# Optimization experiments

Measured on AMD Instinct MI355X. Metric: run time of the kernel, lower is better.

The kernel has to match this reference:

```python
import jax, jax.numpy as jnp
import numpy as np

DIM = 512
HEADS = 8
HD = DIM // HEADS          # head_dim = 64
GROUPS = 32                # GroupNorm groups
EPS = 1e-5
SCALE = HD ** -0.25        # double-scale: applied to both q and k
B, H, W, L, CTX = 8, 32, 32, 77, 768


def setup_inputs() -> dict:
    key = jax.random.key(0)
    ks = jax.random.split(key, 6)
    return {
        "x": jax.random.normal(ks[0], (B, DIM, H, W), jnp.float32),
        "context": jax.random.normal(ks[1], (B, L, CTX), jnp.float32),
        "gn_gamma": jnp.ones((DIM,), jnp.float32),
        "gn_beta": jnp.zeros((DIM,), jnp.float32),
        "qkv_w": jax.random.normal(ks[2], (3 * DIM, DIM), jnp.float32) * 0.02,
        "qkv_b": jnp.zeros((3 * DIM,), jnp.float32),
        "ckv_w": jax.random.normal(ks[3], (2 * DIM, CTX), jnp.float32) * 0.02,
        "ckv_b": jnp.zeros((2 * DIM,), jnp.float32),
        "proj_w": jax.random.normal(ks[4], (DIM, DIM), jnp.float32) * 0.02,
        "proj_b": jnp.zeros((DIM,), jnp.float32),
    }


def _group_norm(x, gamma, beta):
    b, c, h, w = x.shape
    xr = x.reshape(b, GROUPS, c // GROUPS, h, w)
    mu = xr.mean(axis=(2, 3, 4), keepdims=True)
    var = xr.var(axis=(2, 3, 4), keepdims=True)
    xr = (xr - mu) * jax.lax.rsqrt(var + EPS)
    return xr.reshape(b, c, h, w) * gamma[None, :, None, None] + beta[None, :, None, None]


def reference(x, context, gn_gamma, gn_beta, qkv_w, qkv_b, ckv_w, ckv_b, proj_w, proj_b):
    b, c, h, w = x.shape
    n, d = HEADS, HD
    identity = x

    xn = _group_norm(x, gn_gamma, gn_beta)
    # 1x1 conv == channel GEMM. qkv: [b, 3*dim, h*w] -> [b, 3, n, d, hw]
    qkv = jnp.einsum('bchw,oc->bohw', xn, qkv_w) + qkv_b[None, :, None, None]
    qkv = qkv.reshape(b, 3, n, d, h * w)
    q, k, v = qkv[:, 0], qkv[:, 1], qkv[:, 2]   # each [b, n, d, hw]

    # context kv: Linear(context_dim, 2*dim) -> [b, L, 2, n, d] -> [b, n, d, L]
    ckv = jnp.einsum('blc,oc->blo', context, ckv_w) + ckv_b
    ckv = ckv.reshape(b, -1, 2, n, d)
    ck = jnp.transpose(ckv[:, :, 0], (0, 2, 3, 1))  # [b, n, d, L]
    cv = jnp.transpose(ckv[:, :, 1], (0, 2, 3, 1))
    k = jnp.concatenate([ck, k], axis=-1)           # [b, n, d, L+hw]
    v = jnp.concatenate([cv, v], axis=-1)

    # attn = (q^T * s) @ (k * s); softmax over keys
    attn = jnp.einsum('bndq,bndk->bnqk', q * SCALE, k * SCALE)
    attn = jax.nn.softmax(attn, axis=-1)
    out = jnp.einsum('bndk,bnqk->bndq', v, attn).reshape(b, c, h, w)

    out = jnp.einsum('bchw,oc->bohw', out, proj_w) + proj_b[None, :, None, None]
    return out + identity
```

## Files before the change

### kernel.cpp

```cpp
#include <hip/hip_runtime.h>

#define B_ 8
#define DIM_ 512
#define HEADS_ 8
#define HD_ 64
#define HW_ 1024
#define L_ 77
#define LP_ 80
#define CTX_ 768
#define KV_ 1101
#define KVP_ 1152
#define CTX0_ 1024
#define SC_QK 0.42466089f

typedef __attribute__((ext_vector_type(8))) short bf16x8;
typedef __attribute__((ext_vector_type(4))) float f32x4;
typedef __attribute__((ext_vector_type(4))) unsigned short u16x4;

__device__ __forceinline__ unsigned short f2bf(float f) {
  union { float f; unsigned int u; } c; c.f = f;
  unsigned int u = c.u;
  return (unsigned short)((u + 0x7fffu + ((u >> 16) & 1u)) >> 16);
}
__device__ __forceinline__ float bf2f(unsigned short h) {
  union { unsigned int u; float f; } c; c.u = ((unsigned int)h) << 16;
  return c.f;
}

#define GLD_LDS16(gsrc, ldst) \
  __builtin_amdgcn_global_load_lds((const __attribute__((address_space(1))) void*)(gsrc), \
                                   (__attribute__((address_space(3))) void*)(ldst), 16, 0, 0)

__global__ __launch_bounds__(256) void conv_w_k(const float* __restrict__ qkv_w,
                                                const float* __restrict__ ckv_w,
                                                const float* __restrict__ proj_w,
                                                unsigned short* __restrict__ dq,
                                                unsigned short* __restrict__ dc,
                                                unsigned short* __restrict__ dp) {
  int i = blockIdx.x * 256 + threadIdx.x;
  const float* src;
  unsigned short* dst;
  int off;
  if (i < 196608) { src = qkv_w; dst = dq; off = i; }
  else if (i < 393216) { src = ckv_w; dst = dc; off = i - 196608; }
  else { src = proj_w; dst = dp; off = i - 393216; }
  float4 v = *(const float4*)(src + (size_t)off * 4);
  u16x4 o;
  o[0] = f2bf(v.x); o[1] = f2bf(v.y); o[2] = f2bf(v.z); o[3] = f2bf(v.w);
  *(u16x4*)(dst + (size_t)off * 4) = o;
}

__global__ __launch_bounds__(256) void conv_ctx_k(const float* __restrict__ ctx,
                                                  unsigned short* __restrict__ dst) {
  int i = blockIdx.x * 256 + threadIdx.x;
  int total4 = B_ * LP_ * CTX_ / 4;
  if (i >= total4) return;
  int idx = i * 4;
  int b = idx / (LP_ * CTX_);
  int rem = idx - b * (LP_ * CTX_);
  int l = rem / CTX_;
  int c = rem - l * CTX_;
  float4 v = make_float4(0.f, 0.f, 0.f, 0.f);
  if (l < L_) v = *(const float4*)&ctx[((size_t)b * L_ + l) * CTX_ + c];
  u16x4 o;
  o[0] = f2bf(v.x); o[1] = f2bf(v.y); o[2] = f2bf(v.z); o[3] = f2bf(v.w);
  *(u16x4*)(dst + idx) = o;
}

__global__ __launch_bounds__(256) void pad_zero_k(unsigned short* __restrict__ k_s,
                                                  unsigned short* __restrict__ vT) {
  int i = blockIdx.x * 256 + threadIdx.x;
  const int total = 64 * (KVP_ - KV_) * 64;
  if (i >= total) return;
  int bh = i / ((KVP_ - KV_) * 64);
  int rem = i - bh * ((KVP_ - KV_) * 64);
  int row = KV_ + rem / 64;
  int d = rem & 63;
  k_s[((size_t)bh * KVP_ + row) * HD_ + d] = 0;
  vT[((size_t)bh * HD_ + d) * KVP_ + row] = 0;
}

__global__ __launch_bounds__(256) void gnorm_k(const float* __restrict__ x,
                                               const float* __restrict__ gamma,
                                               const float* __restrict__ beta,
                                               unsigned short* __restrict__ xn_t) {
  __shared__ unsigned short xs[16][1032];
  __shared__ float red[8];
  const int tid = threadIdx.x;
  const int b = blockIdx.x >> 5, g = blockIdx.x & 31;
  const float* xp = x + ((size_t)b * DIM_ + g * 16) * HW_;
  float sum = 0.f, ssq = 0.f;
#pragma unroll
  for (int i = 0; i < 16; ++i) {
    float4 v = *(const float4*)&xp[i * HW_ + tid * 4];
    sum += v.x + v.y + v.z + v.w;
    ssq += v.x * v.x + v.y * v.y + v.z * v.z + v.w * v.w;
    xs[i][tid * 4 + 0] = f2bf(v.x);
    xs[i][tid * 4 + 1] = f2bf(v.y);
    xs[i][tid * 4 + 2] = f2bf(v.z);
    xs[i][tid * 4 + 3] = f2bf(v.w);
  }
#pragma unroll
  for (int off = 32; off >= 1; off >>= 1) {
    sum += __shfl_xor(sum, off, 64);
    ssq += __shfl_xor(ssq, off, 64);
  }
  if ((tid & 63) == 0) { red[(tid >> 6) * 2] = sum; red[(tid >> 6) * 2 + 1] = ssq; }
  __syncthreads();
  sum = red[0] + red[2] + red[4] + red[6];
  ssq = red[1] + red[3] + red[5] + red[7];
  float mu = sum * (1.f / 16384.f);
  float rstd = rsqrtf(ssq * (1.f / 16384.f) - mu * mu + 1e-5f);
  float a[16], c[16];
#pragma unroll
  for (int ci = 0; ci < 16; ++ci) {
    float gm = gamma[g * 16 + ci], bt = beta[g * 16 + ci];
    a[ci] = rstd * gm;
    c[ci] = bt - mu * rstd * gm;
  }
#pragma unroll
  for (int t = 0; t < 4; ++t) {
    int hw = tid + t * 256;
    unsigned short tmp[16];
#pragma unroll
    for (int ci = 0; ci < 16; ++ci)
      tmp[ci] = f2bf(bf2f(xs[ci][hw]) * a[ci] + c[ci]);
    unsigned int w[8];
#pragma unroll
    for (int j = 0; j < 8; ++j) w[j] = (unsigned int)tmp[2 * j] | ((unsigned int)tmp[2 * j + 1] << 16);
    unsigned short* dptr = &xn_t[((size_t)b * HW_ + hw) * DIM_ + g * 16];
    *(uint4*)dptr = make_uint4(w[0], w[1], w[2], w[3]);
    *(uint4*)(dptr + 8) = make_uint4(w[4], w[5], w[6], w[7]);
  }
}

template <int MODE, int BM, int BN>
__device__ __forceinline__ void gemm_body(int bid,
                                          const unsigned short* __restrict__ A,
                                          const unsigned short* __restrict__ Bt,
                                          int M, int N, int K,
                                          const float* __restrict__ bias,
                                          unsigned short* __restrict__ out_q,
                                          unsigned short* __restrict__ out_k,
                                          unsigned short* __restrict__ out_v,
                                          const float* __restrict__ xres,
                                          float* __restrict__ outf,
                                          unsigned short* sm) {
  constexpr int MR = BM / 32;
  constexpr int NR = BN / 32;
  constexpr int SLOADS = BM / 32 + BN / 32;
  unsigned short* As0 = sm;
  unsigned short* Bs0 = sm + 2 * BM * 64;
  const int tid = threadIdx.x;
  const int wid = tid >> 6, lane = tid & 63;
  const int lr = lane & 15, lg = lane >> 4;
  const int ntn = N / BN;
  const int tm = bid / ntn, tn = bid - tm * ntn;
  const int m0 = tm * BM, n0 = tn * BN;
  const int wr = wid >> 1, wc = wid & 1;
  f32x4 acc[MR][NR] = {};
  const int nkt = K >> 6;

  auto stage = [&](int bi, int kk) {
#pragma unroll
    for (int i = 0; i < BM / 32; ++i) {
      int c = i * 256 + tid;
      int row = c >> 3, ch = (c & 7) ^ (row & 7);
      GLD_LDS16(A + (size_t)(m0 + row) * K + kk + ch * 8,
                As0 + (size_t)bi * BM * 64 + (size_t)(i * 256 + wid * 64) * 8);
    }
#pragma unroll
    for (int i = 0; i < BN / 32; ++i) {
      int c = i * 256 + tid;
      int row = c >> 3, ch = (c & 7) ^ (row & 7);
      GLD_LDS16(Bt + (size_t)(n0 + row) * K + kk + ch * 8,
                Bs0 + (size_t)bi * BN * 64 + (size_t)(i * 256 + wid * 64) * 8);
    }
  };

  __builtin_amdgcn_sched_barrier(0);
  stage(0, 0);
  __builtin_amdgcn_sched_barrier(0);
  if (nkt > 1) stage(1, 64);
  __builtin_amdgcn_sched_barrier(0);

  for (int kt = 0; kt < nkt; ++kt) {
    if (kt < nkt - 1) {
      if constexpr (SLOADS == 8)      asm volatile("s_waitcnt vmcnt(8)" ::: "memory");
      else if constexpr (SLOADS == 6) asm volatile("s_waitcnt vmcnt(6)" ::: "memory");
      else                            asm volatile("s_waitcnt vmcnt(0)" ::: "memory");
    } else {
      asm volatile("s_waitcnt vmcnt(0)" ::: "memory");
    }
    __builtin_amdgcn_sched_barrier(0);
    __builtin_amdgcn_s_barrier();
    __builtin_amdgcn_sched_barrier(0);
    const unsigned short* Ab = As0 + (kt & 1) * BM * 64;
    const unsigned short* Bb = Bs0 + (kt & 1) * BN * 64;
#pragma unroll
    for (int ks = 0; ks < 2; ++ks) {
      bf16x8 af[MR], bf[NR];
#pragma unroll
      for (int mi = 0; mi < MR; ++mi)
        af[mi] = *(const bf16x8*)&Ab[(wr * (BM / 2) + mi * 16 + lr) * 64 +
                                     (((ks * 4 + lg) ^ (lr & 7)) * 8)];
#pragma unroll
      for (int nj = 0; nj < NR; ++nj)
        bf[nj] = *(const bf16x8*)&Bb[(wc * (BN / 2) + nj * 16 + lr) * 64 +
                                     (((ks * 4 + lg) ^ (lr & 7)) * 8)];
#pragma unroll
      for (int mi = 0; mi < MR; ++mi)
#pragma unroll
        for (int nj = 0; nj < NR; ++nj)
          acc[mi][nj] = __builtin_amdgcn_mfma_f32_16x16x32_bf16(af[mi], bf[nj], acc[mi][nj], 0, 0, 0);
    }
    asm volatile("s_waitcnt lgkmcnt(0)" ::: "memory");
    __builtin_amdgcn_sched_barrier(0);
    __builtin_amdgcn_s_barrier();
    __builtin_amdgcn_sched_barrier(0);
    if (kt + 2 < nkt) stage(kt & 1, (kt + 2) << 6);
  }

  if constexpr (MODE == 0) {
    const int which = n0 >> 9;
    const int bb = m0 >> 10;
    const int qibase = m0 & 1023;
    if (which == 2) {
      uint2* Vt = (uint2*)sm;
#pragma unroll
      for (int mi = 0; mi < MR; ++mi) {
#pragma unroll
        for (int nj = 0; nj < NR; ++nj) {
          int col = wc * 64 + nj * 16 + lr;
          float b = bias[n0 + col];
          unsigned int w0, w1;
          float v0 = acc[mi][nj][0] + b, v1 = acc[mi][nj][1] + b;
          float v2 = acc[mi][nj][2] + b, v3 = acc[mi][nj][3] + b;
          asm("v_cvt_pk_bf16_f32 %0, %1, %2" : "=v"(w0) : "v"(v0), "v"(v1));
          asm("v_cvt_pk_bf16_f32 %0, %1, %2" : "=v"(w1) : "v"(v2), "v"(v3));
          int chunk = (wr * 16 + mi * 4 + lg) ^ (lr * 2);
          Vt[col * 32 + chunk] = make_uint2(w0, w1);
        }
      }
      __syncthreads();
#pragma unroll
      for (int it = 0; it < 8; ++it) {
        int col = wid * 32 + it * 4 + lg;
        uint4 val = *(uint4*)&Vt[col * 32 + ((lr * 2) ^ ((col & 15) * 2))];
        int colg = n0 + col;
        int head = (colg >> 6) & 7, d = colg & 63;
        *(uint4*)&out_v[(((size_t)bb * HEADS_ + head) * HD_ + d) * KVP_ + qibase + lr * 8] = val;
      }
    } else {
      unsigned short* Tq = sm;
#pragma unroll
      for (int mi = 0; mi < MR; ++mi) {
#pragma unroll
        for (int nj = 0; nj < NR; ++nj) {
          int col = wc * 64 + nj * 16 + lr;
          float b = bias[n0 + col];
          int qr = wr * 64 + mi * 16 + lg * 4;
#pragma unroll
          for (int r = 0; r < 4; ++r)
            Tq[(qr + r) * 132 + col] = f2bf((acc[mi][nj][r] + b) * SC_QK);
        }
      }
      __syncthreads();
#pragma unroll
      for (int it = 0; it < 8; ++it) {
        int qi = wid * 32 + it * 4 + lg;
        uint2 lo = *(uint2*)&Tq[qi * 132 + lr * 8];
        uint2 hi = *(uint2*)&Tq[qi * 132 + lr * 8 + 4];
        uint4 val = make_uint4(lo.x, lo.y, hi.x, hi.y);
        int colg = n0 + lr * 8;
        int head = (colg >> 6) & 7, d = colg & 63;
        size_t bh = (size_t)bb * HEADS_ + head;
        if (which == 0)
          *(uint4*)&out_q[(bh * HW_ + qibase + qi) * HD_ + d] = val;
        else
          *(uint4*)&out_k[(bh * KVP_ + qibase + qi) * HD_ + d] = val;
      }
    }
  } else {
#pragma unroll
    for (int mi = 0; mi < MR; ++mi) {
#pragma unroll
      for (int nj = 0; nj < NR; ++nj) {
#pragma unroll
        for (int r = 0; r < 4; ++r) {
          int row = m0 + wr * (BM / 2) + mi * 16 + lg * 4 + r;
          int col = n0 + wc * (BN / 2) + nj * 16 + lr;
          float v = acc[mi][nj][r];
          if (MODE == 1) {
            int bb = row / LP_, l = row - bb * LP_;
            if (l < L_) {
              v += bias[col];
              int which = col >> 9, head = (col >> 6) & 7, d = col & 63;
              size_t bh = (size_t)bb * HEADS_ + head;
              if (which == 0) out_k[(bh * KVP_ + CTX0_ + l) * HD_ + d] = f2bf(v * SC_QK);
              else            out_v[(bh * HD_ + d) * KVP_ + CTX0_ + l] = f2bf(v);
            }
          } else {
            size_t idx = (size_t)(col >> 10) * (DIM_ * HW_) + (size_t)row * HW_ + (col & 1023);
            outf[idx] = v + bias[row] + xres[idx];
          }
        }
      }
    }
  }
}

__global__ __launch_bounds__(256, 2) void gemm_qkv_ckv_k(
    const unsigned short* __restrict__ xn_t, const unsigned short* __restrict__ qkvw,
    const unsigned short* __restrict__ ctx_bf, const unsigned short* __restrict__ ckvw,
    const float* __restrict__ qkv_b, const float* __restrict__ ckv_b,
    unsigned short* __restrict__ q_s, unsigned short* __restrict__ k_s,
    unsigned short* __restrict__ vT) {
  __shared__ unsigned short sm[2 * 256 * 64];
  int bid = blockIdx.x;
  if (bid < 80) {
    gemm_body<1, 64, 128>(bid, ctx_bf, ckvw, 640, 1024, 768, ckv_b,
                          nullptr, k_s, vT, nullptr, nullptr, sm);
  } else {
    int b = bid - 80;
    int b2 = (b & 7) * 96 + (b >> 3);
    gemm_body<0, 128, 128>(b2, xn_t, qkvw, 8192, 1536, 512, qkv_b,
                           q_s, k_s, vT, nullptr, nullptr, sm);
  }
}

__global__ __launch_bounds__(256, 2) void gemm_proj_k(
    const unsigned short* __restrict__ projw, const unsigned short* __restrict__ at_s,
    const float* __restrict__ proj_b, const float* __restrict__ x,
    float* __restrict__ out) {
  __shared__ unsigned short sm[2 * 192 * 64];
  gemm_body<2, 64, 128>(blockIdx.x, projw, at_s, 512, 8192, 512, proj_b,
                        nullptr, nullptr, nullptr, x, out, sm);
}

#define PSTRIDE 72

template <bool MASK>
__device__ __forceinline__ void attn_tile64(const unsigned short* __restrict__ Ksb,
                                            const unsigned short* __restrict__ Vsb,
                                            int krem,
                                            const bf16x8 (&qf)[2],
                                            unsigned short* __restrict__ Pw,
                                            int lr, int lg,
                                            const int (&ro)[4], const int (&koff)[2],
                                            float& lrun, f32x4 (&acc)[4]) {
  f32x4 st[4] = {};
  __builtin_amdgcn_s_setprio(1);
#pragma unroll
  for (int ks = 0; ks < 2; ++ks) {
    bf16x8 kf[4];
#pragma unroll
    for (int t = 0; t < 4; ++t)
      kf[t] = *(const bf16x8*)&Ksb[ro[t] + koff[ks]];
#pragma unroll
    for (int t = 0; t < 4; ++t)
      st[t] = __builtin_amdgcn_mfma_f32_16x16x32_bf16(kf[t], qf[ks], st[t], 0, 0, 0);
  }
  __builtin_amdgcn_s_setprio(0);
  if (MASK) {
#pragma unroll
    for (int t = 0; t < 4; ++t)
#pragma unroll
      for (int r = 0; r < 4; ++r)
        st[t][r] = (t * 16 + lg * 4 + r < krem) ? st[t][r] : -INFINITY;
  }
#pragma unroll
  for (int t = 0; t < 4; ++t)
#pragma unroll
    for (int r = 0; r < 4; ++r) st[t][r] = exp2f(st[t][r]);
  float s0 = (st[0][0] + st[0][1]) + (st[0][2] + st[0][3]);
  float s1 = (st[1][0] + st[1][1]) + (st[1][2] + st[1][3]);
  float s2 = (st[2][0] + st[2][1]) + (st[2][2] + st[2][3]);
  float s3 = (st[3][0] + st[3][1]) + (st[3][2] + st[3][3]);
  float rs = (s0 + s1) + (s2 + s3);
  rs += __shfl_xor(rs, 16, 64);
  rs += __shfl_xor(rs, 32, 64);
  lrun += rs;
#pragma unroll
  for (int t = 0; t < 4; ++t) {
    unsigned int w0, w1;
    asm("v_cvt_pk_bf16_f32 %0, %1, %2" : "=v"(w0) : "v"(st[t][0]), "v"(st[t][1]));
    asm("v_cvt_pk_bf16_f32 %0, %1, %2" : "=v"(w1) : "v"(st[t][2]), "v"(st[t][3]));
    *(uint2*)&Pw[lr * PSTRIDE + t * 16 + lg * 4] = make_uint2(w0, w1);
  }
#pragma unroll
  for (int ks = 0; ks < 2; ++ks) {
    bf16x8 pb = *(const bf16x8*)&Pw[lr * PSTRIDE + ks * 32 + lg * 8];
    __builtin_amdgcn_s_setprio(1);
#pragma unroll
    for (int dt = 0; dt < 4; ++dt) {
      bf16x8 vf = *(const bf16x8*)&Vsb[ro[dt] + koff[ks]];
      acc[dt] = __builtin_amdgcn_mfma_f32_16x16x32_bf16(vf, pb, acc[dt], 0, 0, 0);
    }
    __builtin_amdgcn_s_setprio(0);
  }
}

__global__ __launch_bounds__(512, 4) void attn_k(const unsigned short* __restrict__ q_s,
                                                 const unsigned short* __restrict__ k_s,
                                                 const unsigned short* __restrict__ vT,
                                                 unsigned short* __restrict__ at_s) {
  __shared__ unsigned short Ks[2][4096];
  __shared__ unsigned short Vs[2][4096];
  __shared__ unsigned short Pb[8][16 * PSTRIDE];
  const int tid = threadIdx.x;
  const int wid = tid >> 6, lane = tid & 63;
  const int lr = lane & 15, lg = lane >> 4;
  const int bidx = blockIdx.x;
  const int xcd = bidx & 7, idx = bidx >> 3;
  const int bh = xcd + 8 * (idx >> 3);
  const int qt = idx & 7;
  const int q0 = qt * 128 + wid * 16;
  const unsigned short* qp = q_s + (size_t)bh * HW_ * HD_;
  const unsigned short* kp = k_s + (size_t)bh * KVP_ * HD_;
  const unsigned short* vp = vT + (size_t)bh * HD_ * KVP_;
  unsigned short* Pw = Pb[wid];

  const int srow = lane >> 3;
  const int schunk = (lane & 7) ^ srow;

  auto stage = [&](int bufi, int kk) {
    if (wid < 4) {
#pragma unroll
      for (int jj = 0; jj < 2; ++jj)
        GLD_LDS16(kp + (size_t)(kk + wid * 16 + jj * 8 + srow) * HD_ + schunk * 8,
                  &Ks[bufi][(wid * 2 + jj) * 512]);
    } else {
#pragma unroll
      for (int jj = 0; jj < 2; ++jj)
        GLD_LDS16(vp + (size_t)((wid - 4) * 16 + jj * 8 + srow) * KVP_ + kk + schunk * 8,
                  &Vs[bufi][((wid - 4) * 2 + jj) * 512]);
    }
  };

  int ro[4], koff[2];
#pragma unroll
  for (int t = 0; t < 4; ++t) ro[t] = (t * 16 + lr) * 64;
#pragma unroll
  for (int ks = 0; ks < 2; ++ks) koff[ks] = ((ks * 4 + lg) ^ (lr & 7)) * 8;

  bf16x8 qf[2];
#pragma unroll
  for (int ks = 0; ks < 2; ++ks)
    qf[ks] = *(const bf16x8*)&qp[(size_t)(q0 + lr) * HD_ + ks * 32 + lg * 8];

  f32x4 acc[4] = {};
  float lrun = 0.f;

  __builtin_amdgcn_sched_barrier(0);
  stage(0, 0);
  __builtin_amdgcn_sched_barrier(0);
  stage(1, 64);
  __builtin_amdgcn_sched_barrier(0);

  int cur = 0;
  for (int it = 0; it < 17; ++it) {
    asm volatile("s_waitcnt vmcnt(2)" ::: "memory");
    __builtin_amdgcn_sched_barrier(0);
    __builtin_amdgcn_s_barrier();
    __builtin_amdgcn_sched_barrier(0);
    attn_tile64<false>(Ks[cur], Vs[cur], 64, qf, Pw, lr, lg, ro, koff, lrun, acc);
    asm volatile("s_waitcnt lgkmcnt(0)" ::: "memory");
    __builtin_amdgcn_sched_barrier(0);
    __builtin_amdgcn_s_barrier();
    __builtin_amdgcn_sched_barrier(0);
    if (it < 16) stage(cur, (it + 2) * 64);
    cur ^= 1;
  }
  asm volatile("s_waitcnt vmcnt(0)" ::: "memory");
  __builtin_amdgcn_sched_barrier(0);
  __builtin_amdgcn_s_barrier();
  __builtin_amdgcn_sched_barrier(0);
  attn_tile64<true>(Ks[cur], Vs[cur], KV_ - 17 * 64, qf, Pw, lr, lg, ro, koff, lrun, acc);

  const int bb = bh >> 3, head = bh & 7;
  const float inv = 1.f / lrun;
  const int qi = q0 + lr;
#pragma unroll
  for (int dt = 0; dt < 4; ++dt) {
    u16x4 o;
#pragma unroll
    for (int r = 0; r < 4; ++r) o[r] = f2bf(acc[dt][r] * inv);
    *(u16x4*)&at_s[((size_t)bb * HW_ + qi) * DIM_ + head * HD_ + dt * 16 + lg * 4] = o;
  }
}

extern "C" void kernel_launch(void* const* d_in, const int* in_sizes, int n_in,
                              void* d_out, int out_size, void* d_ws, size_t ws_size,
                              hipStream_t stream) {
  (void)in_sizes; (void)n_in; (void)out_size; (void)ws_size;
  const float* x      = (const float*)d_in[0];
  const float* ctx    = (const float*)d_in[1];
  const float* gng    = (const float*)d_in[2];
  const float* gnb    = (const float*)d_in[3];
  const float* qkv_w  = (const float*)d_in[4];
  const float* qkv_b  = (const float*)d_in[5];
  const float* ckv_w  = (const float*)d_in[6];
  const float* ckv_b  = (const float*)d_in[7];
  const float* proj_w = (const float*)d_in[8];
  const float* proj_b = (const float*)d_in[9];
  float* out = (float*)d_out;

  char* ws = (char*)d_ws;
  size_t off = 0;
  auto alloc = [&](size_t bytes) {
    char* p = ws + off;
    off = (off + bytes + 255) & ~(size_t)255;
    return p;
  };
  unsigned short* xn_t    = (unsigned short*)alloc((size_t)B_ * HW_ * DIM_ * 2);
  unsigned short* ctx_bf  = (unsigned short*)alloc((size_t)B_ * LP_ * CTX_ * 2);
  unsigned short* qkvw_bf = (unsigned short*)alloc((size_t)3 * DIM_ * DIM_ * 2);
  unsigned short* ckvw_bf = (unsigned short*)alloc((size_t)2 * DIM_ * CTX_ * 2);
  unsigned short* projw_bf= (unsigned short*)alloc((size_t)DIM_ * DIM_ * 2);
  unsigned short* q_s     = (unsigned short*)alloc((size_t)64 * HW_ * HD_ * 2);
  unsigned short* k_s     = (unsigned short*)alloc((size_t)64 * KVP_ * HD_ * 2);
  unsigned short* vT      = (unsigned short*)alloc((size_t)64 * HD_ * KVP_ * 2);
  unsigned short* at_s    = (unsigned short*)alloc((size_t)B_ * HW_ * DIM_ * 2);

  conv_w_k<<<1792, 256, 0, stream>>>(qkv_w, ckv_w, proj_w, qkvw_bf, ckvw_bf, projw_bf);
  conv_ctx_k<<<480, 256, 0, stream>>>(ctx, ctx_bf);
  gnorm_k<<<256, 256, 0, stream>>>(x, gng, gnb, xn_t);
  pad_zero_k<<<816, 256, 0, stream>>>(k_s, vT);
  gemm_qkv_ckv_k<<<848, 256, 0, stream>>>(xn_t, qkvw_bf, ctx_bf, ckvw_bf,
                                          qkv_b, ckv_b, q_s, k_s, vT);
  attn_k<<<512, 512, 0, stream>>>(q_s, k_s, vT, at_s);
  gemm_proj_k<<<512, 256, 0, stream>>>(projw_bf, at_s, proj_b, x, out);
}
```

Baseline: 88.36 us.

## Compute softmax row sums via MFMA, drop tail mask, merge prep kernels

Replaces the per-tile VALU row-sum and cross-lane shuffles in attention with an extra MFMA against a vector of bf16 ones, accumulating the denominator on the matrix core. The tail-tile mask is dropped: padded keys are zero, so each contributes exp2(0)=1, and the constant NPAD_ is subtracted from the final sum. The weight conversion, context conversion and pad-zeroing kernels are merged into one launch to cut launch overhead. The trade-off is that the denominator is now summed from bf16-rounded probabilities, and correctness relies on the padding staying exactly zero.

Measured after the change: 75.67 us. 1.17x faster.

```diff
diff --git a/kernel.cpp b/kernel.cpp
--- a/kernel.cpp
+++ b/kernel.cpp
@@ -10,6 +10,7 @@
 #define CTX_ 768
 #define KV_ 1101
 #define KVP_ 1152
+#define NPAD_ 51
 #define CTX0_ 1024
 #define SC_QK 0.42466089f
 
@@ -31,53 +32,51 @@
   __builtin_amdgcn_global_load_lds((const __attribute__((address_space(1))) void*)(gsrc), \
                                    (__attribute__((address_space(3))) void*)(ldst), 16, 0, 0)
 
-__global__ __launch_bounds__(256) void conv_w_k(const float* __restrict__ qkv_w,
-                                                const float* __restrict__ ckv_w,
-                                                const float* __restrict__ proj_w,
-                                                unsigned short* __restrict__ dq,
-                                                unsigned short* __restrict__ dc,
-                                                unsigned short* __restrict__ dp) {
-  int i = blockIdx.x * 256 + threadIdx.x;
-  const float* src;
-  unsigned short* dst;
-  int off;
-  if (i < 196608) { src = qkv_w; dst = dq; off = i; }
-  else if (i < 393216) { src = ckv_w; dst = dc; off = i - 196608; }
-  else { src = proj_w; dst = dp; off = i - 393216; }
-  float4 v = *(const float4*)(src + (size_t)off * 4);
-  u16x4 o;
-  o[0] = f2bf(v.x); o[1] = f2bf(v.y); o[2] = f2bf(v.z); o[3] = f2bf(v.w);
-  *(u16x4*)(dst + (size_t)off * 4) = o;
-}
-
-__global__ __launch_bounds__(256) void conv_ctx_k(const float* __restrict__ ctx,
-                                                  unsigned short* __restrict__ dst) {
-  int i = blockIdx.x * 256 + threadIdx.x;
-  int total4 = B_ * LP_ * CTX_ / 4;
-  if (i >= total4) return;
-  int idx = i * 4;
-  int b = idx / (LP_ * CTX_);
-  int rem = idx - b * (LP_ * CTX_);
-  int l = rem / CTX_;
-  int c = rem - l * CTX_;
-  float4 v = make_float4(0.f, 0.f, 0.f, 0.f);
-  if (l < L_) v = *(const float4*)&ctx[((size_t)b * L_ + l) * CTX_ + c];
-  u16x4 o;
-  o[0] = f2bf(v.x); o[1] = f2bf(v.y); o[2] = f2bf(v.z); o[3] = f2bf(v.w);
-  *(u16x4*)(dst + idx) = o;
-}
-
-__global__ __launch_bounds__(256) void pad_zero_k(unsigned short* __restrict__ k_s,
-                                                  unsigned short* __restrict__ vT) {
-  int i = blockIdx.x * 256 + threadIdx.x;
-  const int total = 64 * (KVP_ - KV_) * 64;
-  if (i >= total) return;
-  int bh = i / ((KVP_ - KV_) * 64);
-  int rem = i - bh * ((KVP_ - KV_) * 64);
-  int row = KV_ + rem / 64;
-  int d = rem & 63;
-  k_s[((size_t)bh * KVP_ + row) * HD_ + d] = 0;
-  vT[((size_t)bh * HD_ + d) * KVP_ + row] = 0;
+__global__ __launch_bounds__(256) void prep_k(const float* __restrict__ qkv_w,
+                                              const float* __restrict__ ckv_w,
+                                              const float* __restrict__ proj_w,
+                                              const float* __restrict__ ctx,
+                                              unsigned short* __restrict__ dq,
+                                              unsigned short* __restrict__ dc,
+                                              unsigned short* __restrict__ dp,
+                                              unsigned short* __restrict__ ctx_bf,
+                                              unsigned short* __restrict__ k_s,
+                                              unsigned short* __restrict__ vT) {
+  int bid = blockIdx.x;
+  int tid = threadIdx.x;
+  if (bid < 1792) {
+    int i = bid * 256 + tid;
+    const float* src;
+    unsigned short* dst;
+    int off;
+    if (i < 196608) { src = qkv_w; dst = dq; off = i; }
+    else if (i < 393216) { src = ckv_w; dst = dc; off = i - 196608; }
+    else { src = proj_w; dst = dp; off = i - 393216; }
+    float4 v = *(const float4*)(src + (size_t)off * 4);
+    u16x4 o;
+    o[0] = f2bf(v.x); o[1] = f2bf(v.y); o[2] = f2bf(v.z); o[3] = f2bf(v.w);
+    *(u16x4*)(dst + (size_t)off * 4) = o;
+  } else if (bid < 2272) {
+    int i = (bid - 1792) * 256 + tid;
+    int idx = i * 4;
+    int b = idx / (LP_ * CTX_);
+    int rem = idx - b * (LP_ * CTX_);
+    int l = rem / CTX_;
+    int c = rem - l * CTX_;
+    float4 v = make_float4(0.f, 0.f, 0.f, 0.f);
+    if (l < L_) v = *(const float4*)&ctx[((size_t)b * L_ + l) * CTX_ + c];
+    u16x4 o;
+    o[0] = f2bf(v.x); o[1] = f2bf(v.y); o[2] = f2bf(v.z); o[3] = f2bf(v.w);
+    *(u16x4*)(ctx_bf + idx) = o;
+  } else {
+    int i = (bid - 2272) * 256 + tid;
+    int bh = i / (NPAD_ * 64);
+    int rem = i - bh * (NPAD_ * 64);
+    int row = KV_ + rem / 64;
+    int d = rem & 63;
+    k_s[((size_t)bh * KVP_ + row) * HD_ + d] = 0;
+    vT[((size_t)bh * HD_ + d) * KVP_ + row] = 0;
+  }
 }
 
 __global__ __launch_bounds__(256) void gnorm_k(const float* __restrict__ x,
@@ -340,15 +339,13 @@
 
 #define PSTRIDE 72
 
-template <bool MASK>
 __device__ __forceinline__ void attn_tile64(const unsigned short* __restrict__ Ksb,
                                             const unsigned short* __restrict__ Vsb,
-                                            int krem,
-                                            const bf16x8 (&qf)[2],
+                                            const bf16x8 (&qf)[2], const bf16x8 ones,
                                             unsigned short* __restrict__ Pw,
                                             int lr, int lg,
                                             const int (&ro)[4], const int (&koff)[2],
-                                            float& lrun, f32x4 (&acc)[4]) {
+                                            f32x4& lacc, f32x4 (&acc)[4]) {
   f32x4 st[4] = {};
   __builtin_amdgcn_s_setprio(1);
 #pragma unroll
@@ -362,25 +359,10 @@
       st[t] = __builtin_amdgcn_mfma_f32_16x16x32_bf16(kf[t], qf[ks], st[t], 0, 0, 0);
   }
   __builtin_amdgcn_s_setprio(0);
-  if (MASK) {
-#pragma unroll
-    for (int t = 0; t < 4; ++t)
-#pragma unroll
-      for (int r = 0; r < 4; ++r)
-        st[t][r] = (t * 16 + lg * 4 + r < krem) ? st[t][r] : -INFINITY;
-  }
 #pragma unroll
   for (int t = 0; t < 4; ++t)
 #pragma unroll
-    for (int r = 0; r < 4; ++r) st[t][r] = exp2f(st[t][r]);
-  float s0 = (st[0][0] + st[0][1]) + (st[0][2] + st[0][3]);
-  float s1 = (st[1][0] + st[1][1]) + (st[1][2] + st[1][3]);
-  float s2 = (st[2][0] + st[2][1]) + (st[2][2] + st[2][3]);
-  float s3 = (st[3][0] + st[3][1]) + (st[3][2] + st[3][3]);
-  float rs = (s0 + s1) + (s2 + s3);
-  rs += __shfl_xor(rs, 16, 64);
-  rs += __shfl_xor(rs, 32, 64);
-  lrun += rs;
+    for (int r = 0; r < 4; ++r) st[t][r] = __builtin_amdgcn_exp2f(st[t][r]);
 #pragma unroll
   for (int t = 0; t < 4; ++t) {
     unsigned int w0, w1;
@@ -392,6 +374,7 @@
   for (int ks = 0; ks < 2; ++ks) {
     bf16x8 pb = *(const bf16x8*)&Pw[lr * PSTRIDE + ks * 32 + lg * 8];
     __builtin_amdgcn_s_setprio(1);
+    lacc = __builtin_amdgcn_mfma_f32_16x16x32_bf16(ones, pb, lacc, 0, 0, 0);
 #pragma unroll
     for (int dt = 0; dt < 4; ++dt) {
       bf16x8 vf = *(const bf16x8*)&Vsb[ro[dt] + koff[ks]];
@@ -449,8 +432,12 @@
   for (int ks = 0; ks < 2; ++ks)
     qf[ks] = *(const bf16x8*)&qp[(size_t)(q0 + lr) * HD_ + ks * 32 + lg * 8];
 
+  bf16x8 ones;
+#pragma unroll
+  for (int j = 0; j < 8; ++j) ones[j] = (short)0x3F80;
+
   f32x4 acc[4] = {};
-  float lrun = 0.f;
+  f32x4 lacc = {};
 
   __builtin_amdgcn_sched_barrier(0);
   stage(0, 0);
@@ -464,7 +451,7 @@
     __builtin_amdgcn_sched_barrier(0);
     __builtin_amdgcn_s_barrier();
     __builtin_amdgcn_sched_barrier(0);
-    attn_tile64<false>(Ks[cur], Vs[cur], 64, qf, Pw, lr, lg, ro, koff, lrun, acc);
+    attn_tile64(Ks[cur], Vs[cur], qf, ones, Pw, lr, lg, ro, koff, lacc, acc);
     asm volatile("s_waitcnt lgkmcnt(0)" ::: "memory");
     __builtin_amdgcn_sched_barrier(0);
     __builtin_amdgcn_s_barrier();
@@ -476,10 +463,10 @@
   __builtin_amdgcn_sched_barrier(0);
   __builtin_amdgcn_s_barrier();
   __builtin_amdgcn_sched_barrier(0);
-  attn_tile64<true>(Ks[cur], Vs[cur], KV_ - 17 * 64, qf, Pw, lr, lg, ro, koff, lrun, acc);
+  attn_tile64(Ks[cur], Vs[cur], qf, ones, Pw, lr, lg, ro, koff, lacc, acc);
 
   const int bb = bh >> 3, head = bh & 7;
-  const float inv = 1.f / lrun;
+  const float inv = 1.f / (lacc[0] - (float)NPAD_);
   const int qi = q0 + lr;
 #pragma unroll
   for (int dt = 0; dt < 4; ++dt) {
@@ -523,10 +510,9 @@
   unsigned short* vT      = (unsigned short*)alloc((size_t)64 * HD_ * KVP_ * 2);
   unsigned short* at_s    = (unsigned short*)alloc((size_t)B_ * HW_ * DIM_ * 2);
 
-  conv_w_k<<<1792, 256, 0, stream>>>(qkv_w, ckv_w, proj_w, qkvw_bf, ckvw_bf, projw_bf);
-  conv_ctx_k<<<480, 256, 0, stream>>>(ctx, ctx_bf);
+  prep_k<<<3088, 256, 0, stream>>>(qkv_w, ckv_w, proj_w, ctx,
+                                   qkvw_bf, ckvw_bf, projw_bf, ctx_bf, k_s, vT);
   gnorm_k<<<256, 256, 0, stream>>>(x, gng, gnb, xn_t);
-  pad_zero_k<<<816, 256, 0, stream>>>(k_s, vT);
   gemm_qkv_ckv_k<<<848, 256, 0, stream>>>(xn_t, qkvw_bf, ctx_bf, ckvw_bf,
                                           qkv_b, ckv_b, q_s, k_s, vT);
   attn_k<<<512, 512, 0, stream>>>(q_s, k_s, vT, at_s);
```
